# Optimization experiments

Hardware: AMD Instinct MI355X
Metric: run time of the kernel (lower is better)

Reference implementation:

```python
import jax, jax.numpy as jnp
import numpy as np

EPS = 1e-8
INV_SQRT = 1.0 / np.sqrt(1.0 + EPS)  # 1/sqrt(|k|+eps), |k|=1 for both hyp and sph


def layernorm(x, w, b, eps=1e-5):
    m = jnp.mean(x, axis=-1, keepdims=True)
    v = jnp.mean((x - m) ** 2, axis=-1, keepdims=True)
    return (x - m) * jax.lax.rsqrt(v + eps) * w + b


def setup_inputs() -> dict:
    key = jax.random.key(0)
    B, S, D, H = 4, 1024, 512, 8
    d = D // H
    FF = 2048
    ks = jax.random.split(key, 12)
    s_attn = 1.0 / np.sqrt(d)
    s_d = 1.0 / np.sqrt(D)
    s_ff = 1.0 / np.sqrt(FF)
    return {
        "x": jax.random.normal(ks[0], (B, S, D), jnp.float32),
        "Wq": jax.random.normal(ks[1], (H, d, d), jnp.float32) * s_attn,
        "Wk": jax.random.normal(ks[2], (H, d, d), jnp.float32) * s_attn,
        "Wv": jax.random.normal(ks[3], (H, d, d), jnp.float32) * s_attn,
        "gw": jnp.ones((H, 3), jnp.float32) / 3.0,
        "temp": jnp.ones((H,), jnp.float32),
        "Wo": jax.random.normal(ks[4], (D, D), jnp.float32) * s_d,
        "bo": jnp.zeros((D,), jnp.float32),
        "ln1_w": jnp.ones((D,), jnp.float32),
        "ln1_b": jnp.zeros((D,), jnp.float32),
        "ln2_w": jnp.ones((D,), jnp.float32),
        "ln2_b": jnp.zeros((D,), jnp.float32),
        "W1": jax.random.normal(ks[5], (FF, D), jnp.float32) * s_d,
        "b1": jnp.zeros((FF,), jnp.float32),
        "W2": jax.random.normal(ks[6], (D, FF), jnp.float32) * s_ff,
        "b2": jnp.zeros((D,), jnp.float32),
    }


def reference(x, Wq, Wk, Wv, gw, temp, Wo, bo, ln1_w, ln1_b, ln2_w, ln2_b, W1, b1, W2, b2):
    B, S, D = x.shape
    H = Wq.shape[0]
    d = D // H

    h = layernorm(x, ln1_w, ln1_b)
    xh = h.reshape(B, S, H, d).transpose(0, 2, 1, 3)  # [B,H,S,d]
    # nn.Linear: y = x @ W^T
    q = jnp.einsum("bhsd,hed->bhse", xh, Wq)
    k = jnp.einsum("bhsd,hed->bhse", xh, Wk)
    v = jnp.einsum("bhsd,hed->bhse", xh, Wv)

    qsq = jnp.sum(q * q, axis=-1)  # [B,H,S] == ||q||^2
    ksq = jnp.sum(k * k, axis=-1)
    qk = jnp.einsum("bhsd,bhtd->bhst", q, k)
    # ||q-k||^2 via expansion (same math as sum(diff^2), avoids [B,H,S,S,d])
    dsq = jnp.maximum(qsq[..., :, None] + ksq[..., None, :] - 2.0 * qk, 0.0)
    euc = jnp.sqrt(dsq + EPS)

    denom = (1.0 - qsq)[..., :, None] * (1.0 - ksq)[..., None, :] + EPS
    cosh_arg = jnp.clip(1.0 + 2.0 * dsq / denom, 1.0, 1e6)
    hyp = jnp.arccosh(cosh_arg) * INV_SQRT

    qn = jnp.sqrt(qsq)
    kn = jnp.sqrt(ksq)
    cos_angle = qk / ((qn + EPS)[..., :, None] * (kn + EPS)[..., None, :])
    cos_angle = jnp.clip(cos_angle, -1.0 + EPS, 1.0 - EPS)
    sph = jnp.arccos(cos_angle) * INV_SQRT

    w = jax.nn.softmax(gw, axis=-1)  # [H,3] per-head geometry mixing
    comb = (
        w[:, 0, None, None] * hyp
        + w[:, 1, None, None] * euc
        + w[:, 2, None, None] * sph
    )
    sim = -comb * temp[None, :, None, None]
    attn = jax.nn.softmax(sim, axis=-1)
    out = jnp.einsum("bhst,bhtd->bhsd", attn, v)
    out = out.transpose(0, 2, 1, 3).reshape(B, S, D)
    attn_out = out @ Wo.T + bo

    x = x + attn_out  # dropout=0 (eval)
    h2 = layernorm(x, ln2_w, ln2_b)
    ff = jax.nn.gelu(h2 @ W1.T + b1, approximate=False) @ W2.T + b2
    return x + ff, w
```

## Files before the change

### kernel.cpp

```cpp
#include <hip/hip_runtime.h>
#include <hip/hip_bf16.h>
#include <math.h>

typedef __attribute__((ext_vector_type(4))) float f32x4;
typedef __attribute__((ext_vector_type(8))) short bf16x8;
typedef unsigned short u16;
typedef unsigned int u32;

typedef f32x4  __attribute__((may_alias)) f32x4a;
typedef bf16x8 __attribute__((may_alias)) bf16x8a;
typedef uint2  __attribute__((may_alias)) uint2a;

__device__ __forceinline__ u16 bfbits(float f) {
  union { __hip_bfloat16 h; u16 u; } cv;
  cv.h = __float2bfloat16(f);
  return cv.u;
}
__device__ __forceinline__ float rcp_r(float x)  { return __builtin_amdgcn_rcpf(x); }
__device__ __forceinline__ float sqrt_r(float x) { return __builtin_amdgcn_sqrtf(x); }
__device__ __forceinline__ float log2_r(float x) { return __builtin_amdgcn_logf(x); }
__device__ __forceinline__ float exp2_r(float x) { return __builtin_amdgcn_exp2f(x); }
__device__ __forceinline__ float rsq_r(float x)  { return __builtin_amdgcn_rsqf(x); }
__device__ __forceinline__ u32 cvt_pk_bf16(float lo, float hi) {
  u32 r;
  asm("v_cvt_pk_bf16_f32 %0, %1, %2" : "=v"(r) : "v"(lo), "v"(hi));
  return r;
}
typedef const __attribute__((address_space(1))) unsigned int* gas_t;
typedef __attribute__((address_space(3))) unsigned int* las_t;
__device__ __forceinline__ void gload_lds16(const u16* g, u16* l) {
  __builtin_amdgcn_global_load_lds((gas_t)g, (las_t)l, 16, 0, 0);
}

__global__ __launch_bounds__(256) void convert_weights(
    const float* __restrict__ wq, const float* __restrict__ wk, const float* __restrict__ wv,
    const float* __restrict__ wo, const float* __restrict__ w1, const float* __restrict__ w2,
    u16* __restrict__ owq, u16* __restrict__ owk, u16* __restrict__ owv,
    u16* __restrict__ owo, u16* __restrict__ ow1, u16* __restrict__ ow2) {
  int i = blockIdx.x * 256 + threadIdx.x;
  const float* src; u16* dst; int base;
  if (i < 8192)        { src = wq; dst = owq; base = 0; }
  else if (i < 16384)  { src = wk; dst = owk; base = 8192; }
  else if (i < 24576)  { src = wv; dst = owv; base = 16384; }
  else if (i < 90112)  { src = wo; dst = owo; base = 24576; }
  else if (i < 352256) { src = w1; dst = ow1; base = 90112; }
  else                 { src = w2; dst = ow2; base = 352256; }
  int li = i - base;
  float4 v = reinterpret_cast<const float4*>(src)[li];
  ushort4 o;
  o.x = bfbits(v.x); o.y = bfbits(v.y); o.z = bfbits(v.z); o.w = bfbits(v.w);
  reinterpret_cast<ushort4*>(dst)[li] = o;
}

__global__ __launch_bounds__(128) void ln_kernel(const float* __restrict__ x,
    const float* __restrict__ w, const float* __restrict__ b, u16* __restrict__ out) {
  int row = blockIdx.x, tid = threadIdx.x;
  float4 v = reinterpret_cast<const float4*>(x + row * 512)[tid];
  float s  = v.x + v.y + v.z + v.w;
  float s2 = v.x*v.x + v.y*v.y + v.z*v.z + v.w*v.w;
  #pragma unroll
  for (int o = 32; o > 0; o >>= 1) { s += __shfl_down(s, o); s2 += __shfl_down(s2, o); }
  __shared__ float sm[4];
  if ((tid & 63) == 0) { sm[(tid >> 6)*2] = s; sm[(tid >> 6)*2 + 1] = s2; }
  __syncthreads();
  float ts = sm[0] + sm[2], ts2 = sm[1] + sm[3];
  float mean = ts * (1.f/512.f);
  float var  = ts2 * (1.f/512.f) - mean*mean;
  float rstd = rsq_r(var + 1e-5f);
  float4 wv = reinterpret_cast<const float4*>(w)[tid];
  float4 bv = reinterpret_cast<const float4*>(b)[tid];
  ushort4 o;
  o.x = bfbits((v.x-mean)*rstd*wv.x + bv.x);
  o.y = bfbits((v.y-mean)*rstd*wv.y + bv.y);
  o.z = bfbits((v.z-mean)*rstd*wv.z + bv.z);
  o.w = bfbits((v.w-mean)*rstd*wv.w + bv.w);
  reinterpret_cast<ushort4*>(out + row * 512)[tid] = o;
}

__global__ __launch_bounds__(256) void qkv_kernel(const u16* __restrict__ h1,
    const u16* __restrict__ wqb, const u16* __restrict__ wkb, const u16* __restrict__ wvb,
    u16* __restrict__ q, u16* __restrict__ k, u16* __restrict__ vt,
    float* __restrict__ qsq, float* __restrict__ qom, float* __restrict__ qrs,
    float* __restrict__ ksq, float* __restrict__ kom, float* __restrict__ krs) {
  int mt = blockIdx.x, head = blockIdx.y;
  int wave = threadIdx.x >> 6, lane = threadIdx.x & 63;
  int lr = lane & 15, lg = lane >> 4;
  int m0 = mt * 64 + wave * 16;
  const u16* xr = h1 + (m0 + lr) * 512 + head * 64 + lg * 8;
  bf16x8 a0 = *reinterpret_cast<const bf16x8a*>(xr);
  bf16x8 a1 = *reinterpret_cast<const bf16x8a*>(xr + 32);
  int m_base = m0 + 4*lg;
  int bq = m_base >> 10;
  int s_base = m_base & 1023;
  int bh = (bq << 3) + head;
  #pragma unroll 1
  for (int mat = 0; mat < 3; ++mat) {
    const u16* W = (mat == 0 ? wqb : mat == 1 ? wkb : wvb) + head * 4096;
    f32x4 acc[4];
    #pragma unroll
    for (int c = 0; c < 4; c++)
      #pragma unroll
      for (int j = 0; j < 4; j++) acc[c][j] = 0.f;
    #pragma unroll
    for (int c = 0; c < 4; c++) {
      const u16* wr = W + (c*16 + lr) * 64 + lg * 8;
      bf16x8 b0 = *reinterpret_cast<const bf16x8a*>(wr);
      bf16x8 b1 = *reinterpret_cast<const bf16x8a*>(wr + 32);
      acc[c] = __builtin_amdgcn_mfma_f32_16x16x32_bf16(a0, b0, acc[c], 0, 0, 0);
      acc[c] = __builtin_amdgcn_mfma_f32_16x16x32_bf16(a1, b1, acc[c], 0, 0, 0);
    }
    if (mat == 2) {
      #pragma unroll
      for (int c = 0; c < 4; c++)
        #pragma unroll
        for (int j = 0; j < 4; j++)
          vt[(bh*64 + c*16 + lr) * 1024 + s_base + j] = bfbits(acc[c][j]);
    } else {
      u16* dst = (mat == 0 ? q : k);
      float* sq = (mat == 0 ? qsq : ksq);
      float* om = (mat == 0 ? qom : kom);
      float* rs = (mat == 0 ? qrs : krs);
      float ss[4] = {0.f, 0.f, 0.f, 0.f};
      #pragma unroll
      for (int c = 0; c < 4; c++)
        #pragma unroll
        for (int j = 0; j < 4; j++) {
          float vv = acc[c][j];
          dst[(bh*1024 + s_base + j) * 64 + c*16 + lr] = bfbits(vv);
          ss[j] += vv * vv;
        }
      #pragma unroll
      for (int j = 0; j < 4; j++) {
        #pragma unroll
        for (int o = 1; o < 16; o <<= 1) ss[j] += __shfl_xor(ss[j], o);
      }
      if (lr == 0) {
        #pragma unroll
        for (int j = 0; j < 4; j++) {
          float v = ss[j];
          int idx = bh*1024 + s_base + j;
          sq[idx] = v;
          om[idx] = rcp_r(1.f - v);
          rs[idx] = rsq_r(v);
        }
      }
    }
  }
}

__global__ __launch_bounds__(256, 8) void attn_kernel(
    const u16* __restrict__ q, const u16* __restrict__ k, const u16* __restrict__ vt,
    const float* __restrict__ qsqA, const float* __restrict__ qomA, const float* __restrict__ qrsA,
    const float* __restrict__ ksqA, const float* __restrict__ komA, const float* __restrict__ krsA,
    const float* __restrict__ gw, const float* __restrict__ temp,
    u16* __restrict__ attnb) {
  int bh = blockIdx.y;
  int b = bh >> 3, head = bh & 7;
  int tid = threadIdx.x;
  int wave = tid >> 6;
  int lane = tid & 63;
  int lr = lane & 15, lg = lane >> 4;
  int q0 = blockIdx.x * 16;

  const u16* qp = q  + bh * 65536;
  const u16* kp = k  + bh * 65536;
  const u16* vp = vt + bh * 65536;
  const float* ksb = ksqA + (bh << 10);
  const float* kob = komA + (bh << 10);
  const float* krb = krsA + (bh << 10);

  __shared__ __align__(16) u16 umem[2560];
  u16* pw = umem + wave * 640;

  float g0 = gw[head*3], g1 = gw[head*3+1], g2 = gw[head*3+2];
  float gm = fmaxf(g0, fmaxf(g1, g2));
  float e0 = __expf(g0-gm), e1 = __expf(g1-gm), e2 = __expf(g2-gm);
  float gi = rcp_r(e0 + e1 + e2);
  float tp = temp[head];
  const float LOG2E = 1.4426950408889634f;
  float chn = -e0*gi*tp;
  float cen = -e1*gi*tp*LOG2E;
  float csn = -e2*gi*tp*LOG2E;

  const u16* qr = qp + (q0 + lr) * 64 + lg * 8;
  bf16x8 aq0 = *reinterpret_cast<const bf16x8a*>(qr);
  bf16x8 aq1 = *reinterpret_cast<const bf16x8a*>(qr + 32);
  float qs  = qsqA[(bh << 10) + q0 + lr];
  float qom = qomA[(bh << 10) + q0 + lr];
  float rqn = qrsA[(bh << 10) + q0 + lr];

  f32x4 acc[4];
  #pragma unroll
  for (int c = 0; c < 4; c++)
    #pragma unroll
    for (int j = 0; j < 4; j++) acc[c][j] = 0.f;
  float psum0 = 0.f, psum1 = 0.f;

  for (int it = 0; it < 8; ++it) {
    int t0 = wave * 256 + it * 32;
    const u16* kr = kp + (t0 + lr) * 64 + lg * 8;
    bf16x8 k00 = *reinterpret_cast<const bf16x8a*>(kr);
    bf16x8 k01 = *reinterpret_cast<const bf16x8a*>(kr + 32);
    bf16x8 k10 = *reinterpret_cast<const bf16x8a*>(kr + 1024);
    bf16x8 k11 = *reinterpret_cast<const bf16x8a*>(kr + 1024 + 32);
    f32x4 s0, s1;
    #pragma unroll
    for (int j = 0; j < 4; j++) { s0[j] = 0.f; s1[j] = 0.f; }
    s0 = __builtin_amdgcn_mfma_f32_16x16x32_bf16(k00, aq0, s0, 0, 0, 0);
    s0 = __builtin_amdgcn_mfma_f32_16x16x32_bf16(k01, aq1, s0, 0, 0, 0);
    s1 = __builtin_amdgcn_mfma_f32_16x16x32_bf16(k10, aq0, s1, 0, 0, 0);
    s1 = __builtin_amdgcn_mfma_f32_16x16x32_bf16(k11, aq1, s1, 0, 0, 0);

    float pv0[4], pv1[4];
    #pragma unroll
    for (int tc = 0; tc < 2; tc++) {
      int tt = t0 + tc*16 + 4*lg;
      f32x4 kq = *reinterpret_cast<const f32x4a*>(ksb + tt);
      f32x4 ko = *reinterpret_cast<const f32x4a*>(kob + tt);
      f32x4 krv = *reinterpret_cast<const f32x4a*>(krb + tt);
      f32x4 sv = tc ? s1 : s0;
      float* pv = tc ? pv1 : pv0;
      #pragma unroll
      for (int j = 0; j < 4; j++) {
        float qk  = sv[j];
        float dsq = fmaxf(fmaf(qk, -2.f, qs + kq[j]), 0.f);
        float euc = sqrt_r(dsq + 1e-8f);
        float u   = (dsq + dsq) * qom * ko[j];
        u = fminf(fmaxf(u, 0.f), 999999.f);
        float hyp2 = log2_r((u + 1.f) + sqrt_r(u * (u + 2.f)));
        float ca = qk * rqn * krv[j];
        ca = fminf(fmaxf(ca, -1.f), 1.f);
        float aa = fabsf(ca);
        float pp = fmaf(aa, -0.0187293f, 0.0742610f);
        pp = fmaf(aa, pp, -0.2121144f);
        pp = fmaf(aa, pp, 1.5707288f);
        float rr = sqrt_r(1.f - aa) * pp;
        float sph = ca < 0.f ? 3.14159265358979f - rr : rr;
        float sim2 = fmaf(chn, hyp2, fmaf(cen, euc, csn * sph));
        float p = exp2_r(sim2);
        if (tc) psum1 += p; else psum0 += p;
        pv[j] = p;
      }
    }
    u32 w0 = cvt_pk_bf16(pv0[0], pv0[1]);
    u32 w1 = cvt_pk_bf16(pv0[2], pv0[3]);
    u32 w2 = cvt_pk_bf16(pv1[0], pv1[1]);
    u32 w3 = cvt_pk_bf16(pv1[2], pv1[3]);
    *reinterpret_cast<uint2a*>(pw + lr*40 + 4*lg)      = make_uint2(w0, w1);
    *reinterpret_cast<uint2a*>(pw + lr*40 + 16 + 4*lg) = make_uint2(w2, w3);
    bf16x8 pa = *reinterpret_cast<const bf16x8a*>(pw + lr*40 + lg*8);
    #pragma unroll
    for (int c = 0; c < 4; c++) {
      bf16x8 av = *reinterpret_cast<const bf16x8a*>(vp + (c*16 + lr)*1024 + t0 + lg*8);
      acc[c] = __builtin_amdgcn_mfma_f32_16x16x32_bf16(av, pa, acc[c], 0, 0, 0);
    }
  }

  float lt = psum0 + psum1;
  lt += __shfl_xor(lt, 16);
  lt += __shfl_xor(lt, 32);

  float* fa = (float*)umem;
  __syncthreads();
  #pragma unroll 1
  for (int s = 1; s <= 3; ++s) {
    if (wave == s) {
      #pragma unroll
      for (int c = 0; c < 4; c++)
        *reinterpret_cast<f32x4a*>(fa + lane*20 + c*4) = acc[c];
      fa[lane*20 + 16] = lt;
    }
    __syncthreads();
    if (wave == 0) {
      #pragma unroll
      for (int c = 0; c < 4; c++)
        acc[c] += *reinterpret_cast<const f32x4a*>(fa + lane*20 + c*4);
      lt += fa[lane*20 + 16];
    }
    __syncthreads();
  }
  if (wave == 0) {
    float rl = rcp_r(lt);
    #pragma unroll
    for (int c = 0; c < 4; c++) {
      ushort4 st;
      st.x = bfbits(acc[c][0]*rl); st.y = bfbits(acc[c][1]*rl);
      st.z = bfbits(acc[c][2]*rl); st.w = bfbits(acc[c][3]*rl);
      *reinterpret_cast<ushort4*>(
          &attnb[(size_t)((b << 10) + q0 + lr) * 512 + head*64 + c*16 + 4*lg]) = st;
    }
  }
}

template<int K, int KS, int BN, int MODE>
__global__ __launch_bounds__(256, 4) void gemm_kernel(
    const u16* __restrict__ X, const u16* __restrict__ W,
    const float* __restrict__ bias, const float* __restrict__ res,
    float* __restrict__ outf, float* __restrict__ outf2, u16* __restrict__ outb,
    const float* __restrict__ gw, float* __restrict__ wout) {
  constexpr int NS = (MODE == 1) ? 2048 : 512;
  constexpr int WN = BN / 2;
  constexpr int NFC = WN / 16;
  __shared__ u16 As[64 * 32];
  __shared__ u16 Bs[BN * 32];
  int tid = threadIdx.x;
  int wave = tid >> 6, lane = tid & 63;
  int lr = lane & 15, lg = lane >> 4;
  int wr = wave >> 1, wc = wave & 1;
  int m0 = blockIdx.x * 64, n0 = blockIdx.y * BN;
  const u16* Xp = X;
  const u16* Wp = W;
  if constexpr (MODE == 3) { Xp += blockIdx.z * (KS/2); Wp += blockIdx.z * (KS/2); }
  f32x4 acc[2][NFC];
  #pragma unroll
  for (int fr = 0; fr < 2; fr++)
    #pragma unroll
    for (int fc = 0; fc < NFC; fc++)
      #pragma unroll
      for (int j = 0; j < 4; j++) acc[fr][fc][j] = 0.f;
  int arow = tid >> 2;
  int acol = ((tid & 3) ^ (arow & 3)) << 3;
  const u16* Ag = Xp + (size_t)(m0 + arow) * KS + acol;
  u16* Al = As + wave * 512;
  const u16* Bg0 = Wp + (size_t)(n0 + arow) * KS + acol;
  u16* Bl0 = Bs + wave * 512;
  const u16* Bg1 = nullptr; u16* Bl1 = nullptr;
  if constexpr (BN == 128) {
    int c1 = 256 + tid, r1 = c1 >> 2;
    int s1 = ((c1 & 3) ^ (r1 & 3)) << 3;
    Bg1 = Wp + (size_t)(n0 + r1) * KS + s1;
    Bl1 = Bs + 2048 + wave * 512;
  }
  int rdcol = ((lg ^ (lr & 3)) << 3);
  for (int k0 = 0; k0 < K; k0 += 32) {
    __syncthreads();
    gload_lds16(Ag + k0, Al);
    if (BN != 32 || tid < 128) gload_lds16(Bg0 + k0, Bl0);
    if constexpr (BN == 128) gload_lds16(Bg1 + k0, Bl1);
    __syncthreads();
    bf16x8 af[2], bfr[NFC];
    #pragma unroll
    for (int fr = 0; fr < 2; fr++)
      af[fr] = *reinterpret_cast<const bf16x8a*>(As + (wr*32 + fr*16 + lr)*32 + rdcol);
    #pragma unroll
    for (int fc = 0; fc < NFC; fc++)
      bfr[fc] = *reinterpret_cast<const bf16x8a*>(Bs + (wc*WN + fc*16 + lr)*32 + rdcol);
    #pragma unroll
    for (int fr = 0; fr < 2; fr++)
      #pragma unroll
      for (int fc = 0; fc < NFC; fc++)
        acc[fr][fc] = __builtin_amdgcn_mfma_f32_16x16x32_bf16(af[fr], bfr[fc], acc[fr][fc], 0, 0, 0);
  }
  float* po = nullptr;
  if constexpr (MODE == 3) po = blockIdx.z ? outf2 : outf;
  #pragma unroll
  for (int fr = 0; fr < 2; fr++)
    #pragma unroll
    for (int fc = 0; fc < NFC; fc++) {
      int col = n0 + wc*WN + fc*16 + lr;
      float bb = (MODE == 3) ? 0.f : bias[col];
      #pragma unroll
      for (int j = 0; j < 4; j++) {
        int row = m0 + wr*32 + fr*16 + 4*lg + j;
        float v = acc[fr][fc][j] + bb;
        if constexpr (MODE == 0) {
          outf[(size_t)row*NS + col] = v + res[(size_t)row*NS + col];
        } else if constexpr (MODE == 1) {
          float t = v * fmaf(v*v, 0.035677408137f, 0.7978845608f);
          float g = v * rcp_r(1.f + exp2_r(-2.8853900817779268f * t));
          outb[(size_t)row*NS + col] = bfbits(g);
        } else {
          po[(size_t)row*512 + col] = v;
        }
      }
    }
  (void)gw; (void)wout;
}

__global__ __launch_bounds__(256) void ff2_combine(
    const float* __restrict__ p0, const float* __restrict__ p1,
    const float* __restrict__ bias, const float* __restrict__ res,
    float* __restrict__ out, const float* __restrict__ gw, float* __restrict__ wout) {
  int i = blockIdx.x * 256 + threadIdx.x;
  float4 a = reinterpret_cast<const float4*>(p0)[i];
  float4 b = reinterpret_cast<const float4*>(p1)[i];
  float4 r = reinterpret_cast<const float4*>(res)[i];
  int col4 = (i & 127) << 2;
  float4 bb = *reinterpret_cast<const float4*>(bias + col4);
  float4 o;
  o.x = a.x + b.x + r.x + bb.x;
  o.y = a.y + b.y + r.y + bb.y;
  o.z = a.z + b.z + r.z + bb.z;
  o.w = a.w + b.w + r.w + bb.w;
  reinterpret_cast<float4*>(out)[i] = o;
  if (blockIdx.x == 0 && threadIdx.x < 8) {
    int h = threadIdx.x;
    float a0 = gw[h*3], a1 = gw[h*3+1], a2 = gw[h*3+2];
    float m = fmaxf(a0, fmaxf(a1, a2));
    float x0 = __expf(a0-m), x1 = __expf(a1-m), x2 = __expf(a2-m);
    float inv = rcp_r(x0 + x1 + x2);
    wout[h*3+0] = x0*inv; wout[h*3+1] = x1*inv; wout[h*3+2] = x2*inv;
  }
}

extern "C" void kernel_launch(void* const* d_in, const int* in_sizes, int n_in,
                              void* d_out, int out_size, void* d_ws, size_t ws_size,
                              hipStream_t stream) {
  const float* x    = (const float*)d_in[0];
  const float* Wq   = (const float*)d_in[1];
  const float* Wk   = (const float*)d_in[2];
  const float* Wv   = (const float*)d_in[3];
  const float* gw   = (const float*)d_in[4];
  const float* temp = (const float*)d_in[5];
  const float* Wo   = (const float*)d_in[6];
  const float* bo   = (const float*)d_in[7];
  const float* ln1w = (const float*)d_in[8];
  const float* ln1b = (const float*)d_in[9];
  const float* ln2w = (const float*)d_in[10];
  const float* ln2b = (const float*)d_in[11];
  const float* W1   = (const float*)d_in[12];
  const float* b1   = (const float*)d_in[13];
  const float* W2   = (const float*)d_in[14];
  const float* b2   = (const float*)d_in[15];

  char* ws = (char*)d_ws;
  u16*  wqb  = (u16*)(ws + 0);
  u16*  wkb  = (u16*)(ws + 65536);
  u16*  wvb  = (u16*)(ws + 131072);
  u16*  wob  = (u16*)(ws + 196608);
  u16*  w1b  = (u16*)(ws + 720896);
  u16*  w2b  = (u16*)(ws + 2818048);
  u16*  h1b  = (u16*)(ws + 4915200);
  u16*  qb   = (u16*)(ws + 9109504);
  u16*  kb   = (u16*)(ws + 13303808);
  u16*  vtb  = (u16*)(ws + 17498112);
  float* qsq = (float*)(ws + 21692416);
  float* ksq = (float*)(ws + 21823488);
  float* qom = (float*)(ws + 21954560);
  float* qrs = (float*)(ws + 22085632);
  float* kom = (float*)(ws + 22216704);
  float* krs = (float*)(ws + 22347776);
  u16*  attnb= (u16*)(ws + 22478848);
  float* x1  = (float*)(ws + 26673152);
  u16*  h2b  = (u16*)(ws + 35061760);
  float* p1f = (float*)(ws + 35061760);
  u16*  gb   = (u16*)(ws + 4915200);

  float* outf = (float*)d_out;
  float* wout = outf + 4096*512;

  convert_weights<<<2400, 256, 0, stream>>>(Wq, Wk, Wv, Wo, W1, W2,
                                            wqb, wkb, wvb, wob, w1b, w2b);
  ln_kernel<<<4096, 128, 0, stream>>>(x, ln1w, ln1b, h1b);
  qkv_kernel<<<dim3(64, 8), 256, 0, stream>>>(h1b, wqb, wkb, wvb, qb, kb, vtb,
                                              qsq, qom, qrs, ksq, kom, krs);
  attn_kernel<<<dim3(64, 32), 256, 0, stream>>>(qb, kb, vtb, qsq, qom, qrs,
                                                ksq, kom, krs, gw, temp, attnb);
  gemm_kernel<512, 512, 32, 0><<<dim3(64, 16), 256, 0, stream>>>(
      attnb, wob, bo, x, x1, nullptr, nullptr, nullptr, nullptr);
  ln_kernel<<<4096, 128, 0, stream>>>(x1, ln2w, ln2b, h2b);
  gemm_kernel<512, 512, 128, 1><<<dim3(64, 16), 256, 0, stream>>>(
      h2b, w1b, b1, nullptr, nullptr, nullptr, gb, nullptr, nullptr);
  gemm_kernel<1024, 2048, 64, 3><<<dim3(64, 8, 2), 256, 0, stream>>>(
      gb, w2b, nullptr, nullptr, outf, p1f, nullptr, nullptr, nullptr);
  ff2_combine<<<2048, 256, 0, stream>>>(outf, p1f, b2, x1, outf, gw, wout);
}
```

Before: 261.3 us.

## Stage key norms in LDS, widen attention blocks, drop precomputed reciprocals

The attention kernel now runs 512-thread blocks that cover 32 queries, with two query groups each split across four key ranges. Per-key squared norms and reciprocal norms are staged once per block in shared memory instead of being re-read from global memory by every wave. The per-row 1/(1-||x||^2) arrays are removed: the hyperbolic denominator is recomputed inline with an rcp, which trades two global arrays for some extra ALU work. The output-projection GEMM also switches to a wider N tile with half as many blocks.

```diff
diff --git a/kernel.cpp b/kernel.cpp
--- a/kernel.cpp
+++ b/kernel.cpp
@@ -80,8 +80,8 @@
 __global__ __launch_bounds__(256) void qkv_kernel(const u16* __restrict__ h1,
     const u16* __restrict__ wqb, const u16* __restrict__ wkb, const u16* __restrict__ wvb,
     u16* __restrict__ q, u16* __restrict__ k, u16* __restrict__ vt,
-    float* __restrict__ qsq, float* __restrict__ qom, float* __restrict__ qrs,
-    float* __restrict__ ksq, float* __restrict__ kom, float* __restrict__ krs) {
+    float* __restrict__ qsq, float* __restrict__ qrs,
+    float* __restrict__ ksq, float* __restrict__ krs) {
   int mt = blockIdx.x, head = blockIdx.y;
   int wave = threadIdx.x >> 6, lane = threadIdx.x & 63;
   int lr = lane & 15, lg = lane >> 4;
@@ -118,7 +118,6 @@
     } else {
       u16* dst = (mat == 0 ? q : k);
       float* sq = (mat == 0 ? qsq : ksq);
-      float* om = (mat == 0 ? qom : kom);
       float* rs = (mat == 0 ? qrs : krs);
       float ss[4] = {0.f, 0.f, 0.f, 0.f};
       #pragma unroll
@@ -140,7 +139,6 @@
           float v = ss[j];
           int idx = bh*1024 + s_base + j;
           sq[idx] = v;
-          om[idx] = rcp_r(1.f - v);
           rs[idx] = rsq_r(v);
         }
       }
@@ -148,29 +146,35 @@
   }
 }
 
-__global__ __launch_bounds__(256, 8) void attn_kernel(
+__global__ __launch_bounds__(512, 6) void attn_kernel(
     const u16* __restrict__ q, const u16* __restrict__ k, const u16* __restrict__ vt,
-    const float* __restrict__ qsqA, const float* __restrict__ qomA, const float* __restrict__ qrsA,
-    const float* __restrict__ ksqA, const float* __restrict__ komA, const float* __restrict__ krsA,
+    const float* __restrict__ qsqA, const float* __restrict__ qrsA,
+    const float* __restrict__ ksqA, const float* __restrict__ krsA,
     const float* __restrict__ gw, const float* __restrict__ temp,
     u16* __restrict__ attnb) {
   int bh = blockIdx.y;
   int b = bh >> 3, head = bh & 7;
   int tid = threadIdx.x;
   int wave = tid >> 6;
+  int wq = wave & 1;
+  int split = wave >> 1;
   int lane = tid & 63;
   int lr = lane & 15, lg = lane >> 4;
-  int q0 = blockIdx.x * 16;
+  int q0 = blockIdx.x * 32 + wq * 16;
 
   const u16* qp = q  + bh * 65536;
   const u16* kp = k  + bh * 65536;
   const u16* vp = vt + bh * 65536;
-  const float* ksb = ksqA + (bh << 10);
-  const float* kob = komA + (bh << 10);
-  const float* krb = krsA + (bh << 10);
-
-  __shared__ __align__(16) u16 umem[2560];
+
+  __shared__ float ks_s[1024], rkn_s[1024];
+  __shared__ __align__(16) u16 umem[5120];
   u16* pw = umem + wave * 640;
+
+  for (int i = tid; i < 1024; i += 512) {
+    ks_s[i]  = ksqA[(bh << 10) + i];
+    rkn_s[i] = krsA[(bh << 10) + i];
+  }
+  __syncthreads();
 
   float g0 = gw[head*3], g1 = gw[head*3+1], g2 = gw[head*3+2];
   float gm = fmaxf(g0, fmaxf(g1, g2));
@@ -186,7 +190,7 @@
   bf16x8 aq0 = *reinterpret_cast<const bf16x8a*>(qr);
   bf16x8 aq1 = *reinterpret_cast<const bf16x8a*>(qr + 32);
   float qs  = qsqA[(bh << 10) + q0 + lr];
-  float qom = qomA[(bh << 10) + q0 + lr];
+  float omq = 1.f - qs;
   float rqn = qrsA[(bh << 10) + q0 + lr];
 
   f32x4 acc[4];
@@ -197,7 +201,7 @@
   float psum0 = 0.f, psum1 = 0.f;
 
   for (int it = 0; it < 8; ++it) {
-    int t0 = wave * 256 + it * 32;
+    int t0 = split * 256 + it * 32;
     const u16* kr = kp + (t0 + lr) * 64 + lg * 8;
     bf16x8 k00 = *reinterpret_cast<const bf16x8a*>(kr);
     bf16x8 k01 = *reinterpret_cast<const bf16x8a*>(kr + 32);
@@ -211,24 +215,29 @@
     s1 = __builtin_amdgcn_mfma_f32_16x16x32_bf16(k10, aq0, s1, 0, 0, 0);
     s1 = __builtin_amdgcn_mfma_f32_16x16x32_bf16(k11, aq1, s1, 0, 0, 0);
 
+    f32x4 kq0 = *reinterpret_cast<const f32x4a*>(&ks_s[t0 + 4*lg]);
+    f32x4 kq1 = *reinterpret_cast<const f32x4a*>(&ks_s[t0 + 16 + 4*lg]);
+    f32x4 rk0 = *reinterpret_cast<const f32x4a*>(&rkn_s[t0 + 4*lg]);
+    f32x4 rk1 = *reinterpret_cast<const f32x4a*>(&rkn_s[t0 + 16 + 4*lg]);
+
     float pv0[4], pv1[4];
     #pragma unroll
     for (int tc = 0; tc < 2; tc++) {
-      int tt = t0 + tc*16 + 4*lg;
-      f32x4 kq = *reinterpret_cast<const f32x4a*>(ksb + tt);
-      f32x4 ko = *reinterpret_cast<const f32x4a*>(kob + tt);
-      f32x4 krv = *reinterpret_cast<const f32x4a*>(krb + tt);
       f32x4 sv = tc ? s1 : s0;
+      f32x4 kq = tc ? kq1 : kq0;
+      f32x4 rk = tc ? rk1 : rk0;
       float* pv = tc ? pv1 : pv0;
       #pragma unroll
       for (int j = 0; j < 4; j++) {
         float qk  = sv[j];
-        float dsq = fmaxf(fmaf(qk, -2.f, qs + kq[j]), 0.f);
+        float ksj = kq[j];
+        float dsq = fmaxf(fmaf(qk, -2.f, qs + ksj), 0.f);
         float euc = sqrt_r(dsq + 1e-8f);
-        float u   = (dsq + dsq) * qom * ko[j];
+        float den = fmaf(omq, 1.f - ksj, 1e-8f);
+        float u   = (dsq + dsq) * rcp_r(den);
         u = fminf(fmaxf(u, 0.f), 999999.f);
         float hyp2 = log2_r((u + 1.f) + sqrt_r(u * (u + 2.f)));
-        float ca = qk * rqn * krv[j];
+        float ca = qk * rqn * rk[j];
         ca = fminf(fmaxf(ca, -1.f), 1.f);
         float aa = fabsf(ca);
         float pp = fmaf(aa, -0.0187293f, 0.0742610f);
@@ -264,22 +273,23 @@
   __syncthreads();
   #pragma unroll 1
   for (int s = 1; s <= 3; ++s) {
-    if (wave == s) {
+    int base = (wq*64 + lane)*20;
+    if (split == s) {
       #pragma unroll
       for (int c = 0; c < 4; c++)
-        *reinterpret_cast<f32x4a*>(fa + lane*20 + c*4) = acc[c];
-      fa[lane*20 + 16] = lt;
+        *reinterpret_cast<f32x4a*>(fa + base + c*4) = acc[c];
+      fa[base + 16] = lt;
     }
     __syncthreads();
-    if (wave == 0) {
+    if (split == 0) {
       #pragma unroll
       for (int c = 0; c < 4; c++)
-        acc[c] += *reinterpret_cast<const f32x4a*>(fa + lane*20 + c*4);
-      lt += fa[lane*20 + 16];
+        acc[c] += *reinterpret_cast<const f32x4a*>(fa + base + c*4);
+      lt += fa[base + 16];
     }
     __syncthreads();
   }
-  if (wave == 0) {
+  if (split == 0) {
     float rl = rcp_r(lt);
     #pragma unroll
     for (int c = 0; c < 4; c++) {
@@ -436,10 +446,8 @@
   u16*  vtb  = (u16*)(ws + 17498112);
   float* qsq = (float*)(ws + 21692416);
   float* ksq = (float*)(ws + 21823488);
-  float* qom = (float*)(ws + 21954560);
-  float* qrs = (float*)(ws + 22085632);
-  float* kom = (float*)(ws + 22216704);
-  float* krs = (float*)(ws + 22347776);
+  float* qrs = (float*)(ws + 21954560);
+  float* krs = (float*)(ws + 22085632);
   u16*  attnb= (u16*)(ws + 22478848);
   float* x1  = (float*)(ws + 26673152);
   u16*  h2b  = (u16*)(ws + 35061760);
@@ -453,10 +461,10 @@
                                             wqb, wkb, wvb, wob, w1b, w2b);
   ln_kernel<<<4096, 128, 0, stream>>>(x, ln1w, ln1b, h1b);
   qkv_kernel<<<dim3(64, 8), 256, 0, stream>>>(h1b, wqb, wkb, wvb, qb, kb, vtb,
-                                              qsq, qom, qrs, ksq, kom, krs);
-  attn_kernel<<<dim3(64, 32), 256, 0, stream>>>(qb, kb, vtb, qsq, qom, qrs,
-                                                ksq, kom, krs, gw, temp, attnb);
-  gemm_kernel<512, 512, 32, 0><<<dim3(64, 16), 256, 0, stream>>>(
+                                              qsq, qrs, ksq, krs);
+  attn_kernel<<<dim3(32, 32), 512, 0, stream>>>(qb, kb, vtb, qsq, qrs,
+                                                ksq, krs, gw, temp, attnb);
+  gemm_kernel<512, 512, 64, 0><<<dim3(64, 8), 256, 0, stream>>>(
       attnb, wob, bo, x, x1, nullptr, nullptr, nullptr, nullptr);
   ln_kernel<<<4096, 128, 0, stream>>>(x1, ln2w, ln2b, h2b);
   gemm_kernel<512, 512, 128, 1><<<dim3(64, 16), 256, 0, stream>>>(
```

Result: faster. 222.9 us (-14.7%).
